# Kernel tuning notes

Hardware: AMD Instinct MI355X
Metric: run time of the kernel (lower is better)

Reference implementation:

```python
import jax, jax.numpy as jnp
import numpy as np

DIM = 1024
K = 7
DILATION = 2
BATCH = 16384
NEG_SLOPE = 0.01


def setup_inputs() -> dict:
    key = jax.random.key(0)
    k1, k2, k3, k4 = jax.random.split(key, 4)
    x = jax.random.normal(k1, (BATCH, DIM), dtype=jnp.float32)
    # Conv1d(1,1,K) default init ~ U(-1/sqrt(K), 1/sqrt(K)); normal is fine for a baseline
    weight = jax.random.normal(k2, (1, 1, K), dtype=jnp.float32) * 0.3
    bias = jax.random.normal(k3, (1,), dtype=jnp.float32) * 0.1
    lmbd = jax.random.normal(k4, (DIM,), dtype=jnp.float32)
    return {"x": x, "weight": weight, "bias": bias, "lmbd": lmbd}


def _forward(x, weight, bias, lmbd):
    pad = (K - 1) * DILATION
    padded = jnp.pad(x, ((0, 0), (0, pad)))  # right-pad last dim
    # (B,1,L) conv with dilated kernel (1,1,K), VALID -> output length = DIM
    conv = jax.lax.conv_general_dilated(
        padded[:, None, :], weight,
        window_strides=(1,), padding="VALID", rhs_dilation=(DILATION,),
        dimension_numbers=("NCH", "OIH", "NCH"))
    conv = conv[:, 0, :] + bias[0]  # (B, DIM)

    w = weight.reshape(-1)  # (K,)
    w0 = w[0]

    activation = jnp.where(conv >= 0, conv, NEG_SLOPE * conv)  # leaky_relu
    act_grad = jnp.where(activation >= 0, 1.0, NEG_SLOPE)

    sp = jax.nn.softplus(lmbd)
    scale = jnp.where(w0 == 0, lmbd,
                      jnp.where(w0 > 0, -1.0 / w0 + sp, -1.0 / w0 - sp))  # (DIM,)

    # diag-matmul == broadcasted per-feature scale
    output = activation * scale + x  # skip connection
    act_grad_scaled = act_grad * scale
    logdet = jnp.log(jnp.abs(act_grad_scaled * w0 + 1.0)).sum(axis=1)  # (B,)
    return output, logdet


def reference(x, weight, bias, lmbd):
    return _forward(x, weight, bias, lmbd)
```

## Files before the change

### kernel.cpp

```cpp
#include <hip/hip_runtime.h>
#include <math.h>

#define DIM 1024
#define KK 7
#define DIL 2
#define BATCH 16384
#define NEG 0.01f
#define ROWS 8
#define RPAD 1040

typedef float floatx4 __attribute__((ext_vector_type(4)));

__device__ __forceinline__ void gload_lds16(const float* g, float* l) {
    __builtin_amdgcn_global_load_lds(
        (const __attribute__((address_space(1))) void*)g,
        (__attribute__((address_space(3))) void*)l,
        16 , 0, 0);
}

__global__ __launch_bounds__(256)
void cnn_flow_fused(const float* __restrict__ x,
                    const float* __restrict__ wgt,
                    const float* __restrict__ bias,
                    const float* __restrict__ lmbd,
                    float* __restrict__ out,
                    float* __restrict__ logdet) {
    const int t    = threadIdx.x;
    const int wv   = t >> 6;
    const int lane = t & 63;
    const int base = t << 2;
    const int row0 = blockIdx.x * ROWS;

    __shared__ float sx[ROWS * RPAD];
    __shared__ float red[ROWS][4];

    {
        const float* g0 = x + (size_t)row0 * DIM + (wv << 8) + (lane << 2);
        float*       l0 = sx + (wv << 8) + (lane << 2);
#pragma unroll
        for (int r = 0; r < ROWS; ++r)
            gload_lds16(g0 + r * DIM, l0 + r * RPAD);
    }
    if (t < ROWS * 4) {
        *reinterpret_cast<float4*>(sx + (t >> 2) * RPAD + DIM + ((t & 3) << 2)) =
            make_float4(0.f, 0.f, 0.f, 0.f);
    }

    float w[KK];
#pragma unroll
    for (int k = 0; k < KK; ++k) w[k] = wgt[k];
    const float w0 = w[0];
    const float bs = bias[0];

    float sc[4], lp[4], ln[4];
    {
        float4 lm = *reinterpret_cast<const float4*>(lmbd + base);
        float lms[4] = {lm.x, lm.y, lm.z, lm.w};
        const float inv = (w0 != 0.0f) ? (-1.0f / w0) : 0.0f;
#pragma unroll
        for (int i = 0; i < 4; ++i) {
            float l  = lms[i];
            float sp = fmaxf(l, 0.0f) + log1pf(expf(-fabsf(l)));
            float scale;
            if (w0 == 0.0f)      scale = l;
            else if (w0 > 0.0f)  scale = inv + sp;
            else                 scale = inv - sp;
            sc[i] = scale;
            lp[i] = logf(fabsf(fmaf(scale,       w0, 1.0f)));
            ln[i] = logf(fabsf(fmaf(NEG * scale, w0, 1.0f)));
        }
    }

    __syncthreads();

#pragma unroll
    for (int r = 0; r < ROWS; ++r) {
        const float* srow = sx + r * RPAD + base;
        float xv[16];
#pragma unroll
        for (int j = 0; j < 4; ++j) {
            float4 v = *reinterpret_cast<const float4*>(srow + 4 * j);
            xv[4 * j + 0] = v.x; xv[4 * j + 1] = v.y;
            xv[4 * j + 2] = v.z; xv[4 * j + 3] = v.w;
        }

        float ld_acc = 0.0f;
        float o[4];
#pragma unroll
        for (int i = 0; i < 4; ++i) {
            float conv = bs;
#pragma unroll
            for (int k = 0; k < KK; ++k)
                conv = fmaf(xv[i + DIL * k], w[k], conv);
            bool pos  = (conv >= 0.0f);
            float act = pos ? conv : NEG * conv;
            o[i]      = fmaf(act, sc[i], xv[i]);
            ld_acc   += pos ? lp[i] : ln[i];
        }
        floatx4 ov; ov.x = o[0]; ov.y = o[1]; ov.z = o[2]; ov.w = o[3];
        __builtin_nontemporal_store(ov,
            reinterpret_cast<floatx4*>(out + (size_t)(row0 + r) * DIM + base));

#pragma unroll
        for (int off = 32; off > 0; off >>= 1)
            ld_acc += __shfl_down(ld_acc, off, 64);
        if (lane == 0) red[r][wv] = ld_acc;
    }

    __syncthreads();
    if (t < ROWS)
        logdet[row0 + t] = (red[t][0] + red[t][1]) + (red[t][2] + red[t][3]);
}

extern "C" void kernel_launch(void* const* d_in, const int* in_sizes, int n_in,
                              void* d_out, int out_size, void* d_ws, size_t ws_size,
                              hipStream_t stream) {
    const float* x    = (const float*)d_in[0];
    const float* wgt  = (const float*)d_in[1];
    const float* bias = (const float*)d_in[2];
    const float* lmbd = (const float*)d_in[3];
    float* out    = (float*)d_out;
    float* logdet = out + (size_t)BATCH * DIM;

    cnn_flow_fused<<<BATCH / ROWS, 256, 0, stream>>>(x, wgt, bias, lmbd, out, logdet);
}
```

Before: 28.53 us.

## Pipeline row loads through triple-buffered LDS with manual vmcnt waits

Instead of loading all eight rows into LDS before computing, the kernel loads rows in pairs into a three-slot ring buffer and prefetches the next pair while computing the current one, synchronizing with explicit s_waitcnt and s_barrier. This shrinks the LDS footprint and aims to overlap global loads with compute and stores. It also switches the output store from nontemporal to a regular store. The hand-written vmcnt counts can be fragile because stores also increment the vector memory counter, which risks extra stalls or ordering mistakes.

```diff
diff --git a/kernel.cpp b/kernel.cpp
--- a/kernel.cpp
+++ b/kernel.cpp
@@ -7,15 +7,13 @@
 #define BATCH 16384
 #define NEG 0.01f
 #define ROWS 8
-#define RPAD 1040
-
-typedef float floatx4 __attribute__((ext_vector_type(4)));
+#define RST 1040
+#define NBUF 3
 
 __device__ __forceinline__ void gload_lds16(const float* g, float* l) {
     __builtin_amdgcn_global_load_lds(
         (const __attribute__((address_space(1))) void*)g,
-        (__attribute__((address_space(3))) void*)l,
-        16 , 0, 0);
+        (__attribute__((address_space(3))) void*)l, 16, 0, 0);
 }
 
 __global__ __launch_bounds__(256)
@@ -31,20 +29,17 @@
     const int base = t << 2;
     const int row0 = blockIdx.x * ROWS;
 
-    __shared__ float sx[ROWS * RPAD];
+    __shared__ float sx[NBUF * 2 * RST];
     __shared__ float red[ROWS][4];
 
-    {
-        const float* g0 = x + (size_t)row0 * DIM + (wv << 8) + (lane << 2);
-        float*       l0 = sx + (wv << 8) + (lane << 2);
-#pragma unroll
-        for (int r = 0; r < ROWS; ++r)
-            gload_lds16(g0 + r * DIM, l0 + r * RPAD);
-    }
-    if (t < ROWS * 4) {
-        *reinterpret_cast<float4*>(sx + (t >> 2) * RPAD + DIM + ((t & 3) << 2)) =
-            make_float4(0.f, 0.f, 0.f, 0.f);
-    }
+    const float* gseg = x + (size_t)row0 * DIM + (wv << 8) + (lane << 2);
+    float*       lseg = sx + (wv << 8) + (lane << 2);
+
+    if (t < NBUF * 2 * 16)
+        sx[(t >> 4) * RST + DIM + (t & 15)] = 0.0f;
+
+    gload_lds16(gseg + 0 * DIM, lseg + 0 * RST);
+    gload_lds16(gseg + 1 * DIM, lseg + 1 * RST);
 
     float w[KK];
 #pragma unroll
@@ -71,40 +66,55 @@
         }
     }
 
-    __syncthreads();
+#pragma unroll
+    for (int k = 0; k < ROWS / 2; ++k) {
+        if (k < ROWS / 2 - 1) {
+            float* lb = sx + ((k + 1) % NBUF) * 2 * RST + (wv << 8) + (lane << 2);
+            gload_lds16(gseg + (2 * k + 2) * DIM, lb);
+            gload_lds16(gseg + (2 * k + 3) * DIM, lb + RST);
+        }
+        if (k == 0)
+            asm volatile("s_waitcnt vmcnt(2) lgkmcnt(0)" ::: "memory");
+        else if (k < ROWS / 2 - 1)
+            asm volatile("s_waitcnt vmcnt(4)" ::: "memory");
+        else
+            asm volatile("s_waitcnt vmcnt(2)" ::: "memory");
+        __builtin_amdgcn_s_barrier();
+
+        const float* buf = sx + (k % NBUF) * 2 * RST;
+#pragma unroll
+        for (int rr = 0; rr < 2; ++rr) {
+            const int r = 2 * k + rr;
+            const float* srow = buf + rr * RST + base;
+            float xv[16];
+#pragma unroll
+            for (int j = 0; j < 4; ++j) {
+                float4 v = *reinterpret_cast<const float4*>(srow + 4 * j);
+                xv[4 * j + 0] = v.x; xv[4 * j + 1] = v.y;
+                xv[4 * j + 2] = v.z; xv[4 * j + 3] = v.w;
+            }
+
+            float ld_acc = 0.0f;
+            float o[4];
+#pragma unroll
+            for (int i = 0; i < 4; ++i) {
+                float conv = bs;
+#pragma unroll
+                for (int kk = 0; kk < KK; ++kk)
+                    conv = fmaf(xv[i + DIL * kk], w[kk], conv);
+                bool pos  = (conv >= 0.0f);
+                float act = pos ? conv : NEG * conv;
+                o[i]      = fmaf(act, sc[i], xv[i]);
+                ld_acc   += pos ? lp[i] : ln[i];
+            }
+            *reinterpret_cast<float4*>(out + (size_t)(row0 + r) * DIM + base) =
+                make_float4(o[0], o[1], o[2], o[3]);
 
 #pragma unroll
-    for (int r = 0; r < ROWS; ++r) {
-        const float* srow = sx + r * RPAD + base;
-        float xv[16];
-#pragma unroll
-        for (int j = 0; j < 4; ++j) {
-            float4 v = *reinterpret_cast<const float4*>(srow + 4 * j);
-            xv[4 * j + 0] = v.x; xv[4 * j + 1] = v.y;
-            xv[4 * j + 2] = v.z; xv[4 * j + 3] = v.w;
+            for (int off = 32; off > 0; off >>= 1)
+                ld_acc += __shfl_down(ld_acc, off, 64);
+            if (lane == 0) red[r][wv] = ld_acc;
         }
-
-        float ld_acc = 0.0f;
-        float o[4];
-#pragma unroll
-        for (int i = 0; i < 4; ++i) {
-            float conv = bs;
-#pragma unroll
-            for (int k = 0; k < KK; ++k)
-                conv = fmaf(xv[i + DIL * k], w[k], conv);
-            bool pos  = (conv >= 0.0f);
-            float act = pos ? conv : NEG * conv;
-            o[i]      = fmaf(act, sc[i], xv[i]);
-            ld_acc   += pos ? lp[i] : ln[i];
-        }
-        floatx4 ov; ov.x = o[0]; ov.y = o[1]; ov.z = o[2]; ov.w = o[3];
-        __builtin_nontemporal_store(ov,
-            reinterpret_cast<floatx4*>(out + (size_t)(row0 + r) * DIM + base));
-
-#pragma unroll
-        for (int off = 32; off > 0; off >>= 1)
-            ld_acc += __shfl_down(ld_acc, off, 64);
-        if (lane == 0) red[r][wv] = ld_acc;
     }
 
     __syncthreads();
```

After: 26.83 us. -6.0%, faster.

## Replace LDS staging with double-buffered direct global loads per row

Applied to the files above, without the earlier changes.

Drops the shared-memory staging of the 8-row tile and instead has each thread load its 16-float window (its own 4 elements plus the halo) straight from global memory, using inline asm dwordx4 loads. The next row is prefetched into a second register buffer, with manual vmcnt waits to overlap loads with compute. This removes LDS traffic and the block-wide barrier. In exchange each input element is read about four times from global memory (cached), and the hand-written waitcnt logic is fragile. The nontemporal output store is also replaced with a plain store.

```diff
diff --git a/kernel.cpp b/kernel.cpp
--- a/kernel.cpp
+++ b/kernel.cpp
@@ -7,15 +7,14 @@
 #define BATCH 16384
 #define NEG 0.01f
 #define ROWS 8
-#define RPAD 1040
 
-typedef float floatx4 __attribute__((ext_vector_type(4)));
+typedef float f4v __attribute__((ext_vector_type(4)));
 
-__device__ __forceinline__ void gload_lds16(const float* g, float* l) {
-    __builtin_amdgcn_global_load_lds(
-        (const __attribute__((address_space(1))) void*)g,
-        (__attribute__((address_space(3))) void*)l,
-        16 , 0, 0);
+__device__ __forceinline__ f4v gload4s(unsigned voff_bytes, const float* sbase) {
+    f4v r;
+    asm volatile("global_load_dwordx4 %0, %1, %2"
+                 : "=v"(r) : "v"(voff_bytes), "s"(sbase) : "memory");
+    return r;
 }
 
 __global__ __launch_bounds__(256)
@@ -31,20 +30,7 @@
     const int base = t << 2;
     const int row0 = blockIdx.x * ROWS;
 
-    __shared__ float sx[ROWS * RPAD];
     __shared__ float red[ROWS][4];
-
-    {
-        const float* g0 = x + (size_t)row0 * DIM + (wv << 8) + (lane << 2);
-        float*       l0 = sx + (wv << 8) + (lane << 2);
-#pragma unroll
-        for (int r = 0; r < ROWS; ++r)
-            gload_lds16(g0 + r * DIM, l0 + r * RPAD);
-    }
-    if (t < ROWS * 4) {
-        *reinterpret_cast<float4*>(sx + (t >> 2) * RPAD + DIM + ((t & 3) << 2)) =
-            make_float4(0.f, 0.f, 0.f, 0.f);
-    }
 
     float w[KK];
 #pragma unroll
@@ -52,10 +38,28 @@
     const float w0 = w[0];
     const float bs = bias[0];
 
+    unsigned voff[4];
+#pragma unroll
+    for (int j = 0; j < 4; ++j) {
+        int f = base + 4 * j;
+        voff[j] = 4u * (unsigned)((f <= DIM - 4) ? f : DIM - 4);
+    }
+
+    f4v lm4 = gload4s(4u * (unsigned)base, lmbd);
+    f4v q[2][4];
+    {
+        const float* r0 = x + (size_t)row0 * DIM;
+        q[0][0] = gload4s(voff[0], r0);
+        q[0][1] = gload4s(voff[1], r0);
+        q[0][2] = gload4s(voff[2], r0);
+        q[0][3] = gload4s(voff[3], r0);
+    }
+    asm volatile("s_waitcnt vmcnt(4)" ::: "memory");
+    __builtin_amdgcn_sched_barrier(0);
+
     float sc[4], lp[4], ln[4];
     {
-        float4 lm = *reinterpret_cast<const float4*>(lmbd + base);
-        float lms[4] = {lm.x, lm.y, lm.z, lm.w};
+        float lms[4] = {lm4.x, lm4.y, lm4.z, lm4.w};
         const float inv = (w0 != 0.0f) ? (-1.0f / w0) : 0.0f;
 #pragma unroll
         for (int i = 0; i < 4; ++i) {
@@ -71,17 +75,30 @@
         }
     }
 
-    __syncthreads();
-
 #pragma unroll
     for (int r = 0; r < ROWS; ++r) {
-        const float* srow = sx + r * RPAD + base;
+        const int cb = r & 1, nb = cb ^ 1;
+        if (r + 1 < ROWS) {
+            const float* rn = x + (size_t)(row0 + r + 1) * DIM;
+            q[nb][0] = gload4s(voff[0], rn);
+            q[nb][1] = gload4s(voff[1], rn);
+            q[nb][2] = gload4s(voff[2], rn);
+            q[nb][3] = gload4s(voff[3], rn);
+        }
+        if      (r == 0)        asm volatile("s_waitcnt vmcnt(4)" ::: "memory");
+        else if (r == ROWS - 1) asm volatile("s_waitcnt vmcnt(1)" ::: "memory");
+        else                    asm volatile("s_waitcnt vmcnt(5)" ::: "memory");
+        __builtin_amdgcn_sched_barrier(0);
+
         float xv[16];
+        xv[0]  = q[cb][0].x; xv[1]  = q[cb][0].y; xv[2]  = q[cb][0].z; xv[3]  = q[cb][0].w;
+        xv[4]  = q[cb][1].x; xv[5]  = q[cb][1].y; xv[6]  = q[cb][1].z; xv[7]  = q[cb][1].w;
+        xv[8]  = q[cb][2].x; xv[9]  = q[cb][2].y; xv[10] = q[cb][2].z; xv[11] = q[cb][2].w;
+        xv[12] = q[cb][3].x; xv[13] = q[cb][3].y; xv[14] = q[cb][3].z; xv[15] = q[cb][3].w;
+        if (base > DIM - 16) {
 #pragma unroll
-        for (int j = 0; j < 4; ++j) {
-            float4 v = *reinterpret_cast<const float4*>(srow + 4 * j);
-            xv[4 * j + 0] = v.x; xv[4 * j + 1] = v.y;
-            xv[4 * j + 2] = v.z; xv[4 * j + 3] = v.w;
+            for (int j = 4; j < 16; ++j)
+                if (base + j >= DIM) xv[j] = 0.0f;
         }
 
         float ld_acc = 0.0f;
@@ -90,16 +107,15 @@
         for (int i = 0; i < 4; ++i) {
             float conv = bs;
 #pragma unroll
-            for (int k = 0; k < KK; ++k)
-                conv = fmaf(xv[i + DIL * k], w[k], conv);
+            for (int kk = 0; kk < KK; ++kk)
+                conv = fmaf(xv[i + DIL * kk], w[kk], conv);
             bool pos  = (conv >= 0.0f);
             float act = pos ? conv : NEG * conv;
             o[i]      = fmaf(act, sc[i], xv[i]);
             ld_acc   += pos ? lp[i] : ln[i];
         }
-        floatx4 ov; ov.x = o[0]; ov.y = o[1]; ov.z = o[2]; ov.w = o[3];
-        __builtin_nontemporal_store(ov,
-            reinterpret_cast<floatx4*>(out + (size_t)(row0 + r) * DIM + base));
+        *reinterpret_cast<float4*>(out + (size_t)(row0 + r) * DIM + base) =
+            make_float4(o[0], o[1], o[2], o[3]);
 
 #pragma unroll
         for (int off = 32; off > 0; off >>= 1)
```

Result: faster. 27.36 us (-4.1%).
